# Performance work log

Measured on AMD Instinct MI355X. Metric: run time of the kernel, lower is better.

Reference implementation:

```python
import jax, jax.numpy as jnp
import numpy as np

SEQ_LEN = 200
BATCH = 32768
H = 4  # LSTM hidden size


def _lstm_layer(x, Wih, Whh, bih, bhh):
    """PyTorch-semantics LSTM layer. x: [B,T,D] -> [B,T,H]. Gate order i,f,g,o."""
    # precompute input contribution for all timesteps: [B,T,4H]
    xg = jnp.einsum('btd,gd->btg', x, Wih) + bih + bhh

    def step(carry, xt):
        h, c = carry
        g = xt + h @ Whh.T  # [B,4H]
        i, f, gg, o = jnp.split(g, 4, axis=-1)
        c = jax.nn.sigmoid(f) * c + jax.nn.sigmoid(i) * jnp.tanh(gg)
        h = jax.nn.sigmoid(o) * jnp.tanh(c)
        return (h, c), h

    B = x.shape[0]
    z = jnp.zeros((B, Whh.shape[1]), x.dtype)
    _, hs = jax.lax.scan(step, (z, z), jnp.swapaxes(xg, 0, 1))  # [T,B,H]
    return jnp.swapaxes(hs, 0, 1)


def _lstm2(x, Wih0, Whh0, bih0, bhh0, Wih1, Whh1, bih1, bhh1):
    h = _lstm_layer(x, Wih0, Whh0, bih0, bhh0)
    return _lstm_layer(h, Wih1, Whh1, bih1, bhh1)


def setup_inputs() -> dict:
    key = jax.random.key(0)
    ks = iter(jax.random.split(key, 64))
    def p(shape, s=0.1):
        return jax.random.normal(next(ks), shape, jnp.float32) * s
    d = {"x": jax.random.normal(next(ks), (BATCH, 2, SEQ_LEN), jnp.float32)}
    for r in ("r0", "r1"):
        d[f"{r}_Wih0"] = p((4 * H, 1)); d[f"{r}_Whh0"] = p((4 * H, H))
        d[f"{r}_bih0"] = p((4 * H,));  d[f"{r}_bhh0"] = p((4 * H,))
        d[f"{r}_Wih1"] = p((4 * H, H)); d[f"{r}_Whh1"] = p((4 * H, H))
        d[f"{r}_bih1"] = p((4 * H,));  d[f"{r}_bhh1"] = p((4 * H,))
    d["Wp"] = p((40, 2 * SEQ_LEN)); d["bp"] = p((40,))
    d["WH"] = p((128, 4 * SEQ_LEN)); d["bH"] = p((128,))
    d["WL"] = p((128, 4 * SEQ_LEN)); d["bL"] = p((128,))
    d["W1"] = p((80, 256)); d["b1"] = p((80,))
    d["W2"] = p((40, 80)); d["b2"] = p((40,))
    d["W3"] = p((1, 80)); d["b3"] = p((1,))
    return d


def reference(x,
              r0_Wih0, r0_Whh0, r0_bih0, r0_bhh0, r0_Wih1, r0_Whh1, r0_bih1, r0_bhh1,
              r1_Wih0, r1_Whh0, r1_bih0, r1_bhh0, r1_Wih1, r1_Whh1, r1_bih1, r1_bhh1,
              Wp, bp, WH, bH, WL, bL, W1, b1, W2, b2, W3, b3):
    B = x.shape[0]
    x_flat = x.reshape(B, 2 * SEQ_LEN)
    other = x_flat @ Wp.T + bp  # [B,40]

    Hx = x[:, 0, :, None]  # [B,T,1]
    Lx = x[:, 1, :, None]
    Hh = _lstm2(Hx, r0_Wih0, r0_Whh0, r0_bih0, r0_bhh0, r0_Wih1, r0_Whh1, r0_bih1, r0_bhh1)
    Lh = _lstm2(Lx, r1_Wih0, r1_Whh0, r1_bih0, r1_bhh0, r1_Wih1, r1_Whh1, r1_bih1, r1_bhh1)
    Hf = jnp.tanh(Hh.reshape(B, 4 * SEQ_LEN) @ WH.T + bH)  # [B,128]
    Lf = jnp.tanh(Lh.reshape(B, 4 * SEQ_LEN) @ WL.T + bL)
    z = jnp.concatenate([Hf, Lf], axis=1)  # [B,256]
    z = jnp.tanh(z @ W1.T + b1)  # [B,80]
    z = jnp.tanh(z @ W2.T + b2)  # [B,40]
    z = jnp.concatenate([z, other], axis=1)  # [B,80]
    return jax.nn.sigmoid(z @ W3.T + b3)  # [B,1]
```

## Files before the change

### kernel.cpp

```cpp
#include <hip/hip_runtime.h>
#include <hip/hip_bf16.h>

#define BATCH 32768
#define TSEQ 200

typedef __attribute__((ext_vector_type(8))) short short8;
typedef __attribute__((ext_vector_type(4))) float floatx4;
typedef __attribute__((ext_vector_type(2))) float f32x2;

__device__ __forceinline__ float fast_sigmoid(float x) {
    return __builtin_amdgcn_rcpf(1.0f + __expf(-x));
}
__device__ __forceinline__ float fast_tanh(float x) {
    float e = __expf(2.0f * x);
    return 1.0f - 2.0f * __builtin_amdgcn_rcpf(e + 1.0f);
}
__device__ __forceinline__ short f2bfs(float v) {
    __hip_bfloat16 h = __float2bfloat16(v);
    return __builtin_bit_cast(short, h);
}
__device__ __forceinline__ f32x2 splat2(float x) { f32x2 v; v[0] = x; v[1] = x; return v; }
__device__ __forceinline__ f32x2 pkfma(f32x2 a, f32x2 b, f32x2 c) {
    return __builtin_elementwise_fma(a, b, c);
}
template <int K>
__device__ __forceinline__ float qb(float v) {
    int i = __builtin_bit_cast(int, v);
    int r = __builtin_amdgcn_update_dpp(i, i, K * 0x55, 0xf, 0xf, false);
    return __builtin_bit_cast(float, r);
}
__device__ __forceinline__ void async16(void* lds, const void* g) {
    __builtin_amdgcn_global_load_lds(
        (const __attribute__((address_space(1))) unsigned int*)g,
        (__attribute__((address_space(3))) unsigned int*)lds, 16, 0, 0);
}

#define WS_HH  0
#define WS_WHB 104857600
#define WS_WLB (WS_WHB + 204800)
#define WS_W1B (WS_WLB + 204800)
#define WS_W2B (WS_W1B + 40960)
#define WS_U   (WS_W2B + 9216)
#define WS_OT  (WS_U + 1616)
#define WS_Z   (WS_OT + 262144)

struct LW { const float* p[16]; };

__global__ __launch_bounds__(256) void k_prep(
    const float* __restrict__ WH, const float* __restrict__ WL,
    const float* __restrict__ W1, const float* __restrict__ W2,
    const float* __restrict__ W3, const float* __restrict__ Wp,
    const float* __restrict__ bp, const float* __restrict__ b3,
    __hip_bfloat16* __restrict__ WHbf, __hip_bfloat16* __restrict__ WLbf,
    __hip_bfloat16* __restrict__ W1bf, __hip_bfloat16* __restrict__ W2bf,
    float* __restrict__ u)
{
    int gid = blockIdx.x * 256 + threadIdx.x;
    WHbf[gid] = __float2bfloat16(WH[gid]);
    WLbf[gid] = __float2bfloat16(WL[gid]);
    if (gid < 20480) W1bf[gid] = __float2bfloat16(W1[gid]);
    if (gid < 4608) {
        int rr = gid / 96, cc = gid - rr * 96;
        float v = (rr < 40 && cc < 80) ? W2[rr * 80 + cc] : 0.0f;
        W2bf[gid] = __float2bfloat16(v);
    }
    if (gid < 400) {
        float a = 0.f;
        for (int j = 0; j < 40; ++j) a = fmaf(W3[40 + j], Wp[j * 400 + gid], a);
        u[gid] = a;
    } else if (gid == 400) {
        float a = b3[0];
        for (int j = 0; j < 40; ++j) a = fmaf(W3[40 + j], bp[j], a);
        u[400] = a;
    }
}

__global__ __launch_bounds__(256) void k_lstm(
    const float* __restrict__ x, LW w, const float* __restrict__ u,
    __hip_bfloat16* __restrict__ hh, float* __restrict__ otherp)
{
    int gid = blockIdx.x * 256 + threadIdx.x;
    int q = gid & 3;
    int group = gid >> 2;
    int b = group & (BATCH - 1);
    int r = group >> 15;

    const float* Wih0 = w.p[r * 8 + 0];
    const float* Whh0 = w.p[r * 8 + 1];
    const float* bih0 = w.p[r * 8 + 2];
    const float* bhh0 = w.p[r * 8 + 3];
    const float* Wih1 = w.p[r * 8 + 4];
    const float* Whh1 = w.p[r * 8 + 5];
    const float* bih1 = w.p[r * 8 + 6];
    const float* bhh1 = w.p[r * 8 + 7];

    f32x2 wx0p[2], bb0p[2], bb1p[2], whh0p[2][4], wih1p[2][4], whh1p[2][4];
#pragma unroll
    for (int p = 0; p < 2; ++p) {
#pragma unroll
        for (int c = 0; c < 2; ++c) {
            int G = 2 * p + c;
            int j = 4 * G + q;
            wx0p[p][c] = Wih0[j];
            bb0p[p][c] = bih0[j] + bhh0[j];
            bb1p[p][c] = bih1[j] + bhh1[j];
#pragma unroll
            for (int k = 0; k < 4; ++k) {
                whh0p[p][k][c] = Whh0[j * 4 + k];
                wih1p[p][k][c] = Wih1[j * 4 + k];
                whh1p[p][k][c] = Whh1[j * 4 + k];
            }
        }
    }

    const float* xp = x + ((size_t)b * 2 + r) * TSEQ;
    const float* up = u + r * TSEQ;
    __hip_bfloat16* hp = hh + ((size_t)r * BATCH + b) * (4 * TSEQ) + q;

    float h0 = 0.f, c0 = 0.f, h1 = 0.f, c1 = 0.f, accO = 0.f;

    for (int tb = 0; tb < TSEQ; tb += 4) {
        float4 xv = *(const float4*)(xp + tb);
        float4 uv = *(const float4*)(up + tb);
        float xa[4] = {xv.x, xv.y, xv.z, xv.w};
        float ua[4] = {uv.x, uv.y, uv.z, uv.w};
#pragma unroll
        for (int j = 0; j < 4; ++j) {
            float xt = xa[j];
            accO = fmaf(xt, ua[j], accO);

            float a0 = qb<0>(h0), a1 = qb<1>(h0), a2 = qb<2>(h0), a3 = qb<3>(h0);
            f32x2 g0 = pkfma(splat2(xt), wx0p[0], bb0p[0]);
            f32x2 g1 = pkfma(splat2(xt), wx0p[1], bb0p[1]);
            g0 = pkfma(whh0p[0][0], splat2(a0), g0); g1 = pkfma(whh0p[1][0], splat2(a0), g1);
            g0 = pkfma(whh0p[0][1], splat2(a1), g0); g1 = pkfma(whh0p[1][1], splat2(a1), g1);
            g0 = pkfma(whh0p[0][2], splat2(a2), g0); g1 = pkfma(whh0p[1][2], splat2(a2), g1);
            g0 = pkfma(whh0p[0][3], splat2(a3), g0); g1 = pkfma(whh0p[1][3], splat2(a3), g1);
            float ig = fast_sigmoid(g0[0]);
            float fg = fast_sigmoid(g0[1]);
            float gg = fast_tanh(g1[0]);
            float og = fast_sigmoid(g1[1]);
            c0 = fmaf(fg, c0, ig * gg);
            h0 = og * fast_tanh(c0);

            float p0 = qb<0>(h0), p1 = qb<1>(h0), p2 = qb<2>(h0), p3 = qb<3>(h0);
            float q0 = qb<0>(h1), q1 = qb<1>(h1), q2 = qb<2>(h1), q3 = qb<3>(h1);
            g0 = bb1p[0]; g1 = bb1p[1];
            g0 = pkfma(wih1p[0][0], splat2(p0), g0); g1 = pkfma(wih1p[1][0], splat2(p0), g1);
            g0 = pkfma(wih1p[0][1], splat2(p1), g0); g1 = pkfma(wih1p[1][1], splat2(p1), g1);
            g0 = pkfma(wih1p[0][2], splat2(p2), g0); g1 = pkfma(wih1p[1][2], splat2(p2), g1);
            g0 = pkfma(wih1p[0][3], splat2(p3), g0); g1 = pkfma(wih1p[1][3], splat2(p3), g1);
            g0 = pkfma(whh1p[0][0], splat2(q0), g0); g1 = pkfma(whh1p[1][0], splat2(q0), g1);
            g0 = pkfma(whh1p[0][1], splat2(q1), g0); g1 = pkfma(whh1p[1][1], splat2(q1), g1);
            g0 = pkfma(whh1p[0][2], splat2(q2), g0); g1 = pkfma(whh1p[1][2], splat2(q2), g1);
            g0 = pkfma(whh1p[0][3], splat2(q3), g0); g1 = pkfma(whh1p[1][3], splat2(q3), g1);
            ig = fast_sigmoid(g0[0]);
            fg = fast_sigmoid(g0[1]);
            gg = fast_tanh(g1[0]);
            og = fast_sigmoid(g1[1]);
            c1 = fmaf(fg, c1, ig * gg);
            h1 = og * fast_tanh(c1);

            hp[(tb + j) * 4] = __float2bfloat16(h1);
        }
    }
    if (q == 0) otherp[(size_t)r * BATCH + b] = accO;
}

__global__ __launch_bounds__(256) void k_gemm(
    const __hip_bfloat16* __restrict__ hh,
    const __hip_bfloat16* __restrict__ WHbf, const __hip_bfloat16* __restrict__ WLbf,
    const float* __restrict__ bH, const float* __restrict__ bL,
    __hip_bfloat16* __restrict__ zws)
{
    __shared__ __hip_bfloat16 As[2][128 * 32];
    __shared__ __hip_bfloat16 Bs[2][128 * 32];
    int tid = threadIdx.x;
    int f = blockIdx.y;
    int m0 = blockIdx.x * 128;
    const __hip_bfloat16* A = hh + (size_t)f * BATCH * 800 + (size_t)m0 * 800;
    const __hip_bfloat16* Wb = f ? WLbf : WHbf;
    const float* bias = f ? bL : bH;

    int wv = tid >> 6, lane = tid & 63, l15 = lane & 15, quad = lane >> 4;
    const __hip_bfloat16* ga = A + (size_t)(tid >> 2) * 800 + (tid & 3) * 8;
    const __hip_bfloat16* gb = Wb + (size_t)(tid >> 2) * 800 + (tid & 3) * 8;

    floatx4 acc[2][8] = {};

#define PREFETCH(kc, buf)                                              \
    do {                                                               \
        __hip_bfloat16* la = &As[buf][wv * 512];                       \
        __hip_bfloat16* lb = &Bs[buf][wv * 512];                       \
        async16(la,        ga + (kc) * 32);                            \
        async16(lb,        gb + (kc) * 32);                            \
        async16(la + 2048, ga + 64 * 800 + (kc) * 32);                 \
        async16(lb + 2048, gb + 64 * 800 + (kc) * 32);                 \
    } while (0)

    PREFETCH(0, 0);
    for (int kc = 0; kc < 25; ++kc) {
        __syncthreads();
        if (kc < 24) PREFETCH(kc + 1, (kc + 1) & 1);
        int buf = kc & 1;
        short8 af0 = *(const short8*)(const void*)&As[buf][(wv * 32 + l15) * 32 + quad * 8];
        short8 af1 = *(const short8*)(const void*)&As[buf][(wv * 32 + 16 + l15) * 32 + quad * 8];
#pragma unroll
        for (int nt = 0; nt < 8; ++nt) {
            short8 bfr = *(const short8*)(const void*)&Bs[buf][(nt * 16 + l15) * 32 + quad * 8];
            acc[0][nt] = __builtin_amdgcn_mfma_f32_16x16x32_bf16(af0, bfr, acc[0][nt], 0, 0, 0);
            acc[1][nt] = __builtin_amdgcn_mfma_f32_16x16x32_bf16(af1, bfr, acc[1][nt], 0, 0, 0);
        }
    }
#undef PREFETCH

    float bv[8];
#pragma unroll
    for (int nt = 0; nt < 8; ++nt) bv[nt] = bias[nt * 16 + l15];
#pragma unroll
    for (int mt = 0; mt < 2; ++mt)
#pragma unroll
        for (int nt = 0; nt < 8; ++nt)
#pragma unroll
            for (int rg = 0; rg < 4; ++rg) {
                int row = m0 + wv * 32 + mt * 16 + quad * 4 + rg;
                int col = f * 128 + nt * 16 + l15;
                zws[(size_t)row * 256 + col] =
                    __float2bfloat16(fast_tanh(acc[mt][nt][rg] + bv[nt]));
            }
}

__global__ __launch_bounds__(256) void k_tail(
    const __hip_bfloat16* __restrict__ zws,
    const __hip_bfloat16* __restrict__ W1bf, const __hip_bfloat16* __restrict__ W2bf,
    const float* __restrict__ b1, const float* __restrict__ b2,
    const float* __restrict__ W3, const float* __restrict__ u,
    const float* __restrict__ otherp, float* __restrict__ out)
{
    __shared__ short z1sh[64 * 104];
    __shared__ float z2sh[64 * 49];
    int tid = threadIdx.x;
    int wv = tid >> 6, lane = tid & 63, l15 = lane & 15, quad = lane >> 4;
    int m0 = blockIdx.x * 64;

    for (int i = tid; i < 64 * 24; i += 256) {
        int rr = i / 24, cc = 80 + (i - rr * 24);
        z1sh[rr * 104 + cc] = 0;
    }

    {
        floatx4 acc[5] = {};
#pragma unroll
        for (int kc = 0; kc < 8; ++kc) {
            short8 af = *(const short8*)(const void*)
                (zws + (size_t)(m0 + wv * 16 + l15) * 256 + kc * 32 + quad * 8);
#pragma unroll
            for (int nt = 0; nt < 5; ++nt) {
                short8 bfr = *(const short8*)(const void*)
                    (W1bf + (size_t)(nt * 16 + l15) * 256 + kc * 32 + quad * 8);
                acc[nt] = __builtin_amdgcn_mfma_f32_16x16x32_bf16(af, bfr, acc[nt], 0, 0, 0);
            }
        }
#pragma unroll
        for (int nt = 0; nt < 5; ++nt) {
            int n = nt * 16 + l15;
            float bb = b1[n];
#pragma unroll
            for (int rg = 0; rg < 4; ++rg) {
                int ml = wv * 16 + quad * 4 + rg;
                z1sh[ml * 104 + n] = f2bfs(fast_tanh(acc[nt][rg] + bb));
            }
        }
    }
    __syncthreads();

    {
        floatx4 acc[3] = {};
#pragma unroll
        for (int kc = 0; kc < 3; ++kc) {
            short8 af = *(const short8*)(const void*)
                &z1sh[(wv * 16 + l15) * 104 + kc * 32 + quad * 8];
#pragma unroll
            for (int nt = 0; nt < 3; ++nt) {
                short8 bfr = *(const short8*)(const void*)
                    (W2bf + (size_t)(nt * 16 + l15) * 96 + kc * 32 + quad * 8);
                acc[nt] = __builtin_amdgcn_mfma_f32_16x16x32_bf16(af, bfr, acc[nt], 0, 0, 0);
            }
        }
#pragma unroll
        for (int nt = 0; nt < 3; ++nt) {
            int n = nt * 16 + l15;
            if (n < 40) {
                float bb = b2[n];
#pragma unroll
                for (int rg = 0; rg < 4; ++rg) {
                    int ml = wv * 16 + quad * 4 + rg;
                    z2sh[ml * 49 + n] = fast_tanh(acc[nt][rg] + bb);
                }
            }
        }
    }
    __syncthreads();

    if (tid < 64) {
        int grow = m0 + tid;
        float s = u[400] + otherp[grow] + otherp[BATCH + grow];
        for (int j = 0; j < 40; ++j) s = fmaf(z2sh[tid * 49 + j], W3[j], s);
        out[grow] = fast_sigmoid(s);
    }
}

extern "C" void kernel_launch(void* const* d_in, const int* in_sizes, int n_in,
                              void* d_out, int out_size, void* d_ws, size_t ws_size,
                              hipStream_t stream)
{
    const float* x = (const float*)d_in[0];
    LW w;
    for (int i = 0; i < 16; ++i) w.p[i] = (const float*)d_in[1 + i];
    const float* Wp = (const float*)d_in[17];
    const float* bp = (const float*)d_in[18];
    const float* WH = (const float*)d_in[19];
    const float* bH = (const float*)d_in[20];
    const float* WL = (const float*)d_in[21];
    const float* bL = (const float*)d_in[22];
    const float* W1 = (const float*)d_in[23];
    const float* b1 = (const float*)d_in[24];
    const float* W2 = (const float*)d_in[25];
    const float* b2 = (const float*)d_in[26];
    const float* W3 = (const float*)d_in[27];
    const float* b3 = (const float*)d_in[28];

    char* ws = (char*)d_ws;
    __hip_bfloat16* hh   = (__hip_bfloat16*)(ws + WS_HH);
    __hip_bfloat16* WHbf = (__hip_bfloat16*)(ws + WS_WHB);
    __hip_bfloat16* WLbf = (__hip_bfloat16*)(ws + WS_WLB);
    __hip_bfloat16* W1bf = (__hip_bfloat16*)(ws + WS_W1B);
    __hip_bfloat16* W2bf = (__hip_bfloat16*)(ws + WS_W2B);
    float* u      = (float*)(ws + WS_U);
    float* otherp = (float*)(ws + WS_OT);
    __hip_bfloat16* zws = (__hip_bfloat16*)(ws + WS_Z);
    float* out = (float*)d_out;

    k_prep<<<400, 256, 0, stream>>>(WH, WL, W1, W2, W3, Wp, bp, b3,
                                    WHbf, WLbf, W1bf, W2bf, u);
    k_lstm<<<1024, 256, 0, stream>>>(x, w, u, hh, otherp);
    k_gemm<<<dim3(256, 2), 256, 0, stream>>>(hh, WHbf, WLbf, bH, bL, zws);
    k_tail<<<512, 256, 0, stream>>>(zws, W1bf, W2bf, b1, b2, W3, u, otherp, out);
}
```

Measured before the change: 364.4 us.

## Fold exp scaling into LSTM weights, batch reciprocals, repack h layout, simplify GEMM

The LSTM weights and biases are pre-scaled by -log2e, or 2·log2e for the tanh gate, so each gate needs only a raw exp2. The four gate reciprocals are computed with a single rcp plus multiplies. The h output layout becomes per-lane contiguous across time, which allows packed 4-element bf16 stores, and the WH/WL columns are permuted to match. The GEMM drops LDS double-buffering and reads A and B fragments straight from global memory with smaller per-wave tiles and twice the blocks. This trades LDS reuse for simpler code, and the shared-reciprocal trick risks overflow or precision loss when products of denominators get large.

```diff
diff --git a/kernel.cpp b/kernel.cpp
--- a/kernel.cpp
+++ b/kernel.cpp
@@ -8,11 +8,19 @@
 typedef __attribute__((ext_vector_type(4))) float floatx4;
 typedef __attribute__((ext_vector_type(2))) float f32x2;
 
+#if __has_builtin(__builtin_amdgcn_exp2f)
+__device__ __forceinline__ float EXP2(float x) { return __builtin_amdgcn_exp2f(x); }
+#else
+__device__ __forceinline__ float EXP2(float x) {
+    float r; asm("v_exp_f32 %0, %1" : "=v"(r) : "v"(x)); return r;
+}
+#endif
+
 __device__ __forceinline__ float fast_sigmoid(float x) {
-    return __builtin_amdgcn_rcpf(1.0f + __expf(-x));
+    return __builtin_amdgcn_rcpf(1.0f + EXP2(-1.4426950408889634f * x));
 }
 __device__ __forceinline__ float fast_tanh(float x) {
-    float e = __expf(2.0f * x);
+    float e = EXP2(2.8853900817779268f * x);
     return 1.0f - 2.0f * __builtin_amdgcn_rcpf(e + 1.0f);
 }
 __device__ __forceinline__ short f2bfs(float v) {
@@ -29,11 +37,17 @@
     int r = __builtin_amdgcn_update_dpp(i, i, K * 0x55, 0xf, 0xf, false);
     return __builtin_bit_cast(float, r);
 }
-__device__ __forceinline__ void async16(void* lds, const void* g) {
-    __builtin_amdgcn_global_load_lds(
-        (const __attribute__((address_space(1))) unsigned int*)g,
-        (__attribute__((address_space(3))) unsigned int*)lds, 16, 0, 0);
-}
+__device__ __forceinline__ void rcp4(float d0, float d1, float d2, float d3,
+                                     float& i0, float& i1, float& i2, float& i3) {
+    float p01 = d0 * d1, p23 = d2 * d3;
+    float r = __builtin_amdgcn_rcpf(p01 * p23);
+    float r01 = r * p23, r23 = r * p01;
+    i0 = r01 * d1; i1 = r01 * d0; i2 = r23 * d3; i3 = r23 * d2;
+}
+
+#define LOG2E 1.4426950408889634f
+#define S_SIG (-1.4426950408889634f)
+#define S_TANH (2.8853900817779268f)
 
 #define WS_HH  0
 #define WS_WHB 104857600
@@ -56,8 +70,11 @@
     float* __restrict__ u)
 {
     int gid = blockIdx.x * 256 + threadIdx.x;
-    WHbf[gid] = __float2bfloat16(WH[gid]);
-    WLbf[gid] = __float2bfloat16(WL[gid]);
+    int n = gid / 800, k = gid - n * 800;
+    int t = k >> 2, q = k & 3;
+    int dst = n * 800 + q * 200 + t;
+    WHbf[dst] = __float2bfloat16(WH[gid]);
+    WLbf[dst] = __float2bfloat16(WL[gid]);
     if (gid < 20480) W1bf[gid] = __float2bfloat16(W1[gid]);
     if (gid < 4608) {
         int rr = gid / 96, cc = gid - rr * 96;
@@ -101,21 +118,22 @@
         for (int c = 0; c < 2; ++c) {
             int G = 2 * p + c;
             int j = 4 * G + q;
-            wx0p[p][c] = Wih0[j];
-            bb0p[p][c] = bih0[j] + bhh0[j];
-            bb1p[p][c] = bih1[j] + bhh1[j];
+            float sc = (G == 2) ? S_TANH : S_SIG;
+            wx0p[p][c] = Wih0[j] * sc;
+            bb0p[p][c] = (bih0[j] + bhh0[j]) * sc;
+            bb1p[p][c] = (bih1[j] + bhh1[j]) * sc;
 #pragma unroll
             for (int k = 0; k < 4; ++k) {
-                whh0p[p][k][c] = Whh0[j * 4 + k];
-                wih1p[p][k][c] = Wih1[j * 4 + k];
-                whh1p[p][k][c] = Whh1[j * 4 + k];
+                whh0p[p][k][c] = Whh0[j * 4 + k] * sc;
+                wih1p[p][k][c] = Wih1[j * 4 + k] * sc;
+                whh1p[p][k][c] = Whh1[j * 4 + k] * sc;
             }
         }
     }
 
     const float* xp = x + ((size_t)b * 2 + r) * TSEQ;
     const float* up = u + r * TSEQ;
-    __hip_bfloat16* hp = hh + ((size_t)r * BATCH + b) * (4 * TSEQ) + q;
+    __hip_bfloat16* hp = hh + ((size_t)r * BATCH + b) * 800 + q * 200;
 
     float h0 = 0.f, c0 = 0.f, h1 = 0.f, c1 = 0.f, accO = 0.f;
 
@@ -124,6 +142,7 @@
         float4 uv = *(const float4*)(up + tb);
         float xa[4] = {xv.x, xv.y, xv.z, xv.w};
         float ua[4] = {uv.x, uv.y, uv.z, uv.w};
+        float hb[4];
 #pragma unroll
         for (int j = 0; j < 4; ++j) {
             float xt = xa[j];
@@ -136,12 +155,17 @@
             g0 = pkfma(whh0p[0][1], splat2(a1), g0); g1 = pkfma(whh0p[1][1], splat2(a1), g1);
             g0 = pkfma(whh0p[0][2], splat2(a2), g0); g1 = pkfma(whh0p[1][2], splat2(a2), g1);
             g0 = pkfma(whh0p[0][3], splat2(a3), g0); g1 = pkfma(whh0p[1][3], splat2(a3), g1);
-            float ig = fast_sigmoid(g0[0]);
-            float fg = fast_sigmoid(g0[1]);
-            float gg = fast_tanh(g1[0]);
-            float og = fast_sigmoid(g1[1]);
-            c0 = fmaf(fg, c0, ig * gg);
-            h0 = og * fast_tanh(c0);
+            float di = 1.0f + EXP2(g0[0]);
+            float df = 1.0f + EXP2(g0[1]);
+            float dt = 1.0f + EXP2(g1[0]);
+            float dn = 1.0f + EXP2(g1[1]);
+            float ig, fg, it_, og;
+            rcp4(di, df, dt, dn, ig, fg, it_, og);
+            float tg = fmaf(-2.0f, it_, 1.0f);
+            c0 = fmaf(fg, c0, ig * tg);
+            float dc0 = 1.0f + EXP2(S_TANH * c0);
+            float th0 = fmaf(-2.0f, __builtin_amdgcn_rcpf(dc0), 1.0f);
+            h0 = og * th0;
 
             float p0 = qb<0>(h0), p1 = qb<1>(h0), p2 = qb<2>(h0), p3 = qb<3>(h0);
             float q0 = qb<0>(h1), q1 = qb<1>(h1), q2 = qb<2>(h1), q3 = qb<3>(h1);
@@ -154,15 +178,24 @@
             g0 = pkfma(whh1p[0][1], splat2(q1), g0); g1 = pkfma(whh1p[1][1], splat2(q1), g1);
             g0 = pkfma(whh1p[0][2], splat2(q2), g0); g1 = pkfma(whh1p[1][2], splat2(q2), g1);
             g0 = pkfma(whh1p[0][3], splat2(q3), g0); g1 = pkfma(whh1p[1][3], splat2(q3), g1);
-            ig = fast_sigmoid(g0[0]);
-            fg = fast_sigmoid(g0[1]);
-            gg = fast_tanh(g1[0]);
-            og = fast_sigmoid(g1[1]);
-            c1 = fmaf(fg, c1, ig * gg);
-            h1 = og * fast_tanh(c1);
-
-            hp[(tb + j) * 4] = __float2bfloat16(h1);
-        }
+            di = 1.0f + EXP2(g0[0]);
+            df = 1.0f + EXP2(g0[1]);
+            dt = 1.0f + EXP2(g1[0]);
+            dn = 1.0f + EXP2(g1[1]);
+            rcp4(di, df, dt, dn, ig, fg, it_, og);
+            tg = fmaf(-2.0f, it_, 1.0f);
+            c1 = fmaf(fg, c1, ig * tg);
+            float dc1 = 1.0f + EXP2(S_TANH * c1);
+            float th1 = fmaf(-2.0f, __builtin_amdgcn_rcpf(dc1), 1.0f);
+            h1 = og * th1;
+            hb[j] = h1;
+        }
+        ushort4 pk;
+        pk.x = (unsigned short)f2bfs(hb[0]);
+        pk.y = (unsigned short)f2bfs(hb[1]);
+        pk.z = (unsigned short)f2bfs(hb[2]);
+        pk.w = (unsigned short)f2bfs(hb[3]);
+        *(ushort4*)(hp + tb) = pk;
     }
     if (q == 0) otherp[(size_t)r * BATCH + b] = accO;
 }
@@ -173,61 +206,40 @@
     const float* __restrict__ bH, const float* __restrict__ bL,
     __hip_bfloat16* __restrict__ zws)
 {
-    __shared__ __hip_bfloat16 As[2][128 * 32];
-    __shared__ __hip_bfloat16 Bs[2][128 * 32];
     int tid = threadIdx.x;
     int f = blockIdx.y;
-    int m0 = blockIdx.x * 128;
-    const __hip_bfloat16* A = hh + (size_t)f * BATCH * 800 + (size_t)m0 * 800;
+    int wv = tid >> 6, lane = tid & 63, l15 = lane & 15, quad = lane >> 4;
+    int m0 = blockIdx.x * 64 + wv * 16;
+
     const __hip_bfloat16* Wb = f ? WLbf : WHbf;
     const float* bias = f ? bL : bH;
-
-    int wv = tid >> 6, lane = tid & 63, l15 = lane & 15, quad = lane >> 4;
-    const __hip_bfloat16* ga = A + (size_t)(tid >> 2) * 800 + (tid & 3) * 8;
-    const __hip_bfloat16* gb = Wb + (size_t)(tid >> 2) * 800 + (tid & 3) * 8;
-
-    floatx4 acc[2][8] = {};
-
-#define PREFETCH(kc, buf)                                              \
-    do {                                                               \
-        __hip_bfloat16* la = &As[buf][wv * 512];                       \
-        __hip_bfloat16* lb = &Bs[buf][wv * 512];                       \
-        async16(la,        ga + (kc) * 32);                            \
-        async16(lb,        gb + (kc) * 32);                            \
-        async16(la + 2048, ga + 64 * 800 + (kc) * 32);                 \
-        async16(lb + 2048, gb + 64 * 800 + (kc) * 32);                 \
-    } while (0)
-
-    PREFETCH(0, 0);
+    const short8* ap = (const short8*)(const void*)
+        (hh + (size_t)f * BATCH * 800 + (size_t)(m0 + l15) * 800 + quad * 8);
+    const short8* bp0 = (const short8*)(const void*)
+        (Wb + (size_t)l15 * 800 + quad * 8);
+
+    floatx4 acc[8] = {};
+#pragma unroll 2
     for (int kc = 0; kc < 25; ++kc) {
-        __syncthreads();
-        if (kc < 24) PREFETCH(kc + 1, (kc + 1) & 1);
-        int buf = kc & 1;
-        short8 af0 = *(const short8*)(const void*)&As[buf][(wv * 32 + l15) * 32 + quad * 8];
-        short8 af1 = *(const short8*)(const void*)&As[buf][(wv * 32 + 16 + l15) * 32 + quad * 8];
+        short8 af = ap[kc * 4];
 #pragma unroll
         for (int nt = 0; nt < 8; ++nt) {
-            short8 bfr = *(const short8*)(const void*)&Bs[buf][(nt * 16 + l15) * 32 + quad * 8];
-            acc[0][nt] = __builtin_amdgcn_mfma_f32_16x16x32_bf16(af0, bfr, acc[0][nt], 0, 0, 0);
-            acc[1][nt] = __builtin_amdgcn_mfma_f32_16x16x32_bf16(af1, bfr, acc[1][nt], 0, 0, 0);
-        }
-    }
-#undef PREFETCH
-
-    float bv[8];
-#pragma unroll
-    for (int nt = 0; nt < 8; ++nt) bv[nt] = bias[nt * 16 + l15];
-#pragma unroll
-    for (int mt = 0; mt < 2; ++mt)
-#pragma unroll
-        for (int nt = 0; nt < 8; ++nt)
-#pragma unroll
-            for (int rg = 0; rg < 4; ++rg) {
-                int row = m0 + wv * 32 + mt * 16 + quad * 4 + rg;
-                int col = f * 128 + nt * 16 + l15;
-                zws[(size_t)row * 256 + col] =
-                    __float2bfloat16(fast_tanh(acc[mt][nt][rg] + bv[nt]));
-            }
+            short8 bfr = bp0[(size_t)nt * 1600 + kc * 4];
+            acc[nt] = __builtin_amdgcn_mfma_f32_16x16x32_bf16(af, bfr, acc[nt], 0, 0, 0);
+        }
+    }
+
+#pragma unroll
+    for (int nt = 0; nt < 8; ++nt) {
+        int n = nt * 16 + l15;
+        float bb = bias[n];
+#pragma unroll
+        for (int rg = 0; rg < 4; ++rg) {
+            int row = m0 + quad * 4 + rg;
+            zws[(size_t)row * 256 + f * 128 + n] =
+                __float2bfloat16(fast_tanh(acc[nt][rg] + bb));
+        }
+    }
 }
 
 __global__ __launch_bounds__(256) void k_tail(
@@ -344,6 +356,6 @@
     k_prep<<<400, 256, 0, stream>>>(WH, WL, W1, W2, W3, Wp, bp, b3,
                                     WHbf, WLbf, W1bf, W2bf, u);
     k_lstm<<<1024, 256, 0, stream>>>(x, w, u, hh, otherp);
-    k_gemm<<<dim3(256, 2), 256, 0, stream>>>(hh, WHbf, WLbf, bH, bL, zws);
+    k_gemm<<<dim3(512, 2), 256, 0, stream>>>(hh, WHbf, WLbf, bH, bL, zws);
     k_tail<<<512, 256, 0, stream>>>(zws, W1bf, W2bf, b1, b2, W3, u, otherp, out);
 }
```

New measurement: 469.5 us. +28.8%, slower.
